# Kernel optimization log

Hardware: AMD Instinct MI355X
Metric: run time of the kernel (lower is better)

The kernel has to match this reference:

```python
import jax, jax.numpy as jnp
import numpy as np

N_ITEM_TYPE = 18
N_ITEM_FEAT = 11
N_TYPE_HIDDEN = 32
N_ITEM_HIDDEN = 128
BS, NA, NI = 32, 128, 128


def setup_inputs() -> dict:
    key = jax.random.key(0)
    k1, k2, k3, k4 = jax.random.split(key, 4)
    item_type = jax.random.randint(k1, (BS, NA, NI), 0, N_ITEM_TYPE, dtype=jnp.int64)
    item = jax.random.normal(k2, (BS, NA, NI, N_ITEM_FEAT), dtype=jnp.float32)
    emb = jax.random.normal(k3, (N_ITEM_TYPE, N_TYPE_HIDDEN), dtype=jnp.float32)
    W = jax.random.normal(k4, (N_TYPE_HIDDEN + N_ITEM_FEAT, N_ITEM_HIDDEN), dtype=jnp.float32) * 0.1
    b = jnp.zeros((N_ITEM_HIDDEN,), dtype=jnp.float32)
    return {"item_type": item_type, "item": item, "emb": emb, "W": W, "b": b}


def reference(item_type, item, emb, W, b):
    # embedding gather: [bs, na, ni, 32]
    h_type = emb[item_type]
    # concat features: [bs, na, ni, 43]
    h = jnp.concatenate([h_type, item], axis=-1)
    # Linear + ReLU: [bs, na, ni, n_item_hidden]
    h = jax.nn.relu(jnp.einsum("bnif,fh->bnih", h, W) + b)
    # max-pool over item axis: [bs, na, n_item_hidden]
    return jnp.max(h, axis=2)
```

## Files before the change

### kernel.cpp

```cpp
#include <hip/hip_runtime.h>
#include <hip/hip_bf16.h>
#include <stdint.h>


#define NITEM 128
#define NFEAT 11
#define NTH   32
#define NH    128
#define KREAL 43
#define KSTEPS 3

typedef __attribute__((ext_vector_type(8))) _Float16 half8;
typedef __attribute__((ext_vector_type(16))) float   f32x16;

__global__ __launch_bounds__(64) void prep_b(const float* __restrict__ W,
                                             _Float16* __restrict__ Bpre) {
    const int frag = blockIdx.x;
    const int kk   = frag >> 2;
    const int n    = frag & 3;
    const int lane = threadIdx.x;
    const int col  = n * 32 + (lane & 31);
    const int k0   = kk * 16 + (lane >> 5) * 8;
    half8 pk;
    #pragma unroll
    for (int q = 0; q < 8; ++q) {
        const int k = k0 + q;
        pk[q] = (_Float16)((k < KREAL) ? W[k * NH + col] : 0.0f);
    }
    ((half8*)Bpre)[frag * 64 + lane] = pk;
}

__global__ __launch_bounds__(256, 3) void item_encoder(
    const int*      __restrict__ item_type,
    const float*    __restrict__ item,
    const float*    __restrict__ emb,
    const _Float16* __restrict__ Bpre,
    const float*    __restrict__ bias,
    float*          __restrict__ out)
{
    __shared__ _Float16 Alds[NITEM][64];
    __shared__ float    partial[4][NH];

    const int bn   = blockIdx.x;
    const int t    = threadIdx.x;
    const int lane = t & 63;
    const int w    = t >> 6;
    const int l31  = lane & 31;
    const int lhi  = lane >> 5;

    half8 bf[KSTEPS][4];
    #pragma unroll
    for (int kk = 0; kk < KSTEPS; ++kk)
        #pragma unroll
        for (int n = 0; n < 4; ++n)
            bf[kk][n] = ((const half8*)Bpre)[(kk * 4 + n) * 64 + lane];

    const int*   tyrow = item_type + bn * NITEM;
    const float* itrow = item + (size_t)bn * NITEM * NFEAT;

    #pragma unroll
    for (int j = 0; j < 3; ++j) {
        const int idx = j * 256 + t;
        const int kb  = idx >> 7;
        const int row = idx & 127;
        half8 pk;
        if (kb < 4) {
            const int    ty = tyrow[row];
            const float4 e0 = *(const float4*)(emb + ty * NTH + kb * 8);
            const float4 e1 = *(const float4*)(emb + ty * NTH + kb * 8 + 4);
            pk[0] = (_Float16)e0.x; pk[1] = (_Float16)e0.y;
            pk[2] = (_Float16)e0.z; pk[3] = (_Float16)e0.w;
            pk[4] = (_Float16)e1.x; pk[5] = (_Float16)e1.y;
            pk[6] = (_Float16)e1.z; pk[7] = (_Float16)e1.w;
        } else if (kb == 4) {
            const float* p = itrow + row * NFEAT;
            #pragma unroll
            for (int q = 0; q < 8; ++q) pk[q] = (_Float16)p[q];
        } else {
            const float* p = itrow + row * NFEAT + 8;
            #pragma unroll
            for (int q = 0; q < 8; ++q) pk[q] = (_Float16)((q < 3) ? p[q] : 0.0f);
        }
        ((half8*)&Alds[row][0])[kb ^ (row & 7)] = pk;
    }

    __syncthreads();

    f32x16 acc[4];
    #pragma unroll
    for (int n = 0; n < 4; ++n)
        #pragma unroll
        for (int r = 0; r < 16; ++r) acc[n][r] = 0.0f;

    const int arow = w * 32 + l31;
    #pragma unroll
    for (int kk = 0; kk < KSTEPS; ++kk) {
        const int blk = kk * 2 + lhi;
        const half8 af = ((const half8*)&Alds[arow][0])[blk ^ (arow & 7)];
        #pragma unroll
        for (int n = 0; n < 4; ++n)
            acc[n] = __builtin_amdgcn_mfma_f32_32x32x16_f16(af, bf[kk][n], acc[n], 0, 0, 0);
    }

    #pragma unroll
    for (int n = 0; n < 4; ++n) {
        float m = acc[n][0];
        #pragma unroll
        for (int r = 1; r < 16; ++r) m = fmaxf(m, acc[n][r]);
        m = fmaxf(m, __shfl_xor(m, 32));
        m = fmaxf(m + bias[n * 32 + l31], 0.0f);
        if (lane < 32) partial[w][n * 32 + l31] = m;
    }

    __syncthreads();

    if (t < NH) {
        float m = fmaxf(fmaxf(partial[0][t], partial[1][t]),
                        fmaxf(partial[2][t], partial[3][t]));
        out[(size_t)bn * NH + t] = m;
    }
}

extern "C" void kernel_launch(void* const* d_in, const int* in_sizes, int n_in,
                              void* d_out, int out_size, void* d_ws, size_t ws_size,
                              hipStream_t stream) {
    const int*   item_type = (const int*)  d_in[0];
    const float* item      = (const float*)d_in[1];
    const float* emb       = (const float*)d_in[2];
    const float* W         = (const float*)d_in[3];
    const float* bias      = (const float*)d_in[4];
    float*       out       = (float*)d_out;
    _Float16*    Bpre      = (_Float16*)d_ws;

    prep_b<<<12, 64, 0, stream>>>(W, Bpre);
    item_encoder<<<32 * 128, 256, 0, stream>>>(item_type, item, emb, Bpre, bias, out);
}
```

Baseline: 95.75 us.

## Process four rows per block with coalesced float4 slab staging

Each block now handles four (batch, agent) rows. It stages the whole item-feature slab and the type indices into LDS with coalesced float4/int4 loads. MFMA A fragments are then built straight in registers from the emb gather and the LDS slab, using packed fp16 conversion, so the swizzled fp16 LDS tile is gone. The goal is to replace the strided per-element global feature loads and cut the per-block launch and B-fragment load overhead. In exchange, each block uses more LDS, occupancy drops from 3 to 2 blocks per CU, there are fewer blocks in the grid, and the four rows inside a block run serially.

Measured after the change: 91.07 us. -4.9%, faster.

```diff
diff --git a/kernel.cpp b/kernel.cpp
--- a/kernel.cpp
+++ b/kernel.cpp
@@ -3,15 +3,20 @@
 #include <stdint.h>
 
 
-#define NITEM 128
-#define NFEAT 11
-#define NTH   32
-#define NH    128
-#define KREAL 43
+#define NITEM  128
+#define NFEAT  11
+#define NTH    32
+#define NH     128
+#define KREAL  43
 #define KSTEPS 3
+#define BNPB   4
+#define SLABDW (NITEM * NFEAT)
 
-typedef __attribute__((ext_vector_type(8))) _Float16 half8;
-typedef __attribute__((ext_vector_type(16))) float   f32x16;
+typedef __attribute__((ext_vector_type(8)))  _Float16 half8;
+typedef __attribute__((ext_vector_type(2)))  __fp16   fp16x2;
+typedef __attribute__((ext_vector_type(16))) float    f32x16;
+
+union H8 { half8 h8; fp16x2 h2[4]; };
 
 __global__ __launch_bounds__(64) void prep_b(const float* __restrict__ W,
                                              _Float16* __restrict__ Bpre) {
@@ -30,7 +35,7 @@
     ((half8*)Bpre)[frag * 64 + lane] = pk;
 }
 
-__global__ __launch_bounds__(256, 3) void item_encoder(
+__global__ __launch_bounds__(256, 2) void item_encoder(
     const int*      __restrict__ item_type,
     const float*    __restrict__ item,
     const float*    __restrict__ emb,
@@ -38,15 +43,16 @@
     const float*    __restrict__ bias,
     float*          __restrict__ out)
 {
-    __shared__ _Float16 Alds[NITEM][64];
-    __shared__ float    partial[4][NH];
+    __shared__ float slab[BNPB * SLABDW];
+    __shared__ int   typs[BNPB * NITEM];
+    __shared__ float partial[BNPB][4][NH];
 
-    const int bn   = blockIdx.x;
     const int t    = threadIdx.x;
     const int lane = t & 63;
     const int w    = t >> 6;
     const int l31  = lane & 31;
     const int lhi  = lane >> 5;
+    const int bn0  = blockIdx.x * BNPB;
 
     half8 bf[KSTEPS][4];
     #pragma unroll
@@ -55,69 +61,90 @@
         for (int n = 0; n < 4; ++n)
             bf[kk][n] = ((const half8*)Bpre)[(kk * 4 + n) * 64 + lane];
 
-    const int*   tyrow = item_type + bn * NITEM;
-    const float* itrow = item + (size_t)bn * NITEM * NFEAT;
+    {
+        const float4* gsl = (const float4*)(item + (size_t)bn0 * SLABDW);
+        float4*       lsl = (float4*)slab;
+        #pragma unroll
+        for (int j = 0; j < 5; ++j) lsl[t + 256 * j] = gsl[t + 256 * j];
+        if (t < 128) lsl[1280 + t] = gsl[1280 + t];
+        if (t < 128)
+            ((int4*)typs)[t] = ((const int4*)(item_type + (size_t)bn0 * NITEM))[t];
+    }
+    __syncthreads();
 
+    const int r = w * 32 + l31;
+    float bias4[4];
     #pragma unroll
-    for (int j = 0; j < 3; ++j) {
-        const int idx = j * 256 + t;
-        const int kb  = idx >> 7;
-        const int row = idx & 127;
-        half8 pk;
-        if (kb < 4) {
-            const int    ty = tyrow[row];
-            const float4 e0 = *(const float4*)(emb + ty * NTH + kb * 8);
-            const float4 e1 = *(const float4*)(emb + ty * NTH + kb * 8 + 4);
-            pk[0] = (_Float16)e0.x; pk[1] = (_Float16)e0.y;
-            pk[2] = (_Float16)e0.z; pk[3] = (_Float16)e0.w;
-            pk[4] = (_Float16)e1.x; pk[5] = (_Float16)e1.y;
-            pk[6] = (_Float16)e1.z; pk[7] = (_Float16)e1.w;
-        } else if (kb == 4) {
-            const float* p = itrow + row * NFEAT;
+    for (int n = 0; n < 4; ++n) bias4[n] = bias[n * 32 + l31];
+
+    #pragma unroll 1
+    for (int b = 0; b < BNPB; ++b) {
+        const int    ty = typs[b * NITEM + r];
+        const float* eb = emb + ty * NTH;
+
+        const float4 e0 = *(const float4*)(eb + lhi * 8);
+        const float4 e1 = *(const float4*)(eb + lhi * 8 + 4);
+        const float4 e2 = *(const float4*)(eb + 16 + lhi * 8);
+        const float4 e3 = *(const float4*)(eb + 16 + lhi * 8 + 4);
+
+        H8 a0, a1, a2;
+        a0.h2[0] = __builtin_amdgcn_cvt_pkrtz(e0.x, e0.y);
+        a0.h2[1] = __builtin_amdgcn_cvt_pkrtz(e0.z, e0.w);
+        a0.h2[2] = __builtin_amdgcn_cvt_pkrtz(e1.x, e1.y);
+        a0.h2[3] = __builtin_amdgcn_cvt_pkrtz(e1.z, e1.w);
+        a1.h2[0] = __builtin_amdgcn_cvt_pkrtz(e2.x, e2.y);
+        a1.h2[1] = __builtin_amdgcn_cvt_pkrtz(e2.z, e2.w);
+        a1.h2[2] = __builtin_amdgcn_cvt_pkrtz(e3.x, e3.y);
+        a1.h2[3] = __builtin_amdgcn_cvt_pkrtz(e3.z, e3.w);
+
+        const float* sp = slab + b * SLABDW + r * NFEAT;
+        float fv[8];
+        #pragma unroll
+        for (int q = 0; q < 8; ++q) {
+            const int f  = lhi * 8 + q;
+            const bool ok = (f < NFEAT);
+            const float x = sp[ok ? f : 0];
+            fv[q] = ok ? x : 0.0f;
+        }
+        a2.h2[0] = __builtin_amdgcn_cvt_pkrtz(fv[0], fv[1]);
+        a2.h2[1] = __builtin_amdgcn_cvt_pkrtz(fv[2], fv[3]);
+        a2.h2[2] = __builtin_amdgcn_cvt_pkrtz(fv[4], fv[5]);
+        a2.h2[3] = __builtin_amdgcn_cvt_pkrtz(fv[6], fv[7]);
+
+        f32x16 acc[4];
+        #pragma unroll
+        for (int n = 0; n < 4; ++n)
             #pragma unroll
-            for (int q = 0; q < 8; ++q) pk[q] = (_Float16)p[q];
-        } else {
-            const float* p = itrow + row * NFEAT + 8;
+            for (int rr = 0; rr < 16; ++rr) acc[n][rr] = 0.0f;
+
+        #pragma unroll
+        for (int n = 0; n < 4; ++n) acc[n] = __builtin_amdgcn_mfma_f32_32x32x16_f16(a0.h8, bf[0][n], acc[n], 0, 0, 0);
+        #pragma unroll
+        for (int n = 0; n < 4; ++n) acc[n] = __builtin_amdgcn_mfma_f32_32x32x16_f16(a1.h8, bf[1][n], acc[n], 0, 0, 0);
+        #pragma unroll
+        for (int n = 0; n < 4; ++n) acc[n] = __builtin_amdgcn_mfma_f32_32x32x16_f16(a2.h8, bf[2][n], acc[n], 0, 0, 0);
+
+        #pragma unroll
+        for (int n = 0; n < 4; ++n) {
+            float m = acc[n][0];
             #pragma unroll
-            for (int q = 0; q < 8; ++q) pk[q] = (_Float16)((q < 3) ? p[q] : 0.0f);
+            for (int rr = 1; rr < 16; ++rr) m = fmaxf(m, acc[n][rr]);
+            m = fmaxf(m, __shfl_xor(m, 32));
+            m = fmaxf(m + bias4[n], 0.0f);
+            if (lane < 32) partial[b][w][n * 32 + l31] = m;
         }
-        ((half8*)&Alds[row][0])[kb ^ (row & 7)] = pk;
     }
 
     __syncthreads();
 
-    f32x16 acc[4];
     #pragma unroll
-    for (int n = 0; n < 4; ++n)
-        #pragma unroll
-        for (int r = 0; r < 16; ++r) acc[n][r] = 0.0f;
-
-    const int arow = w * 32 + l31;
-    #pragma unroll
-    for (int kk = 0; kk < KSTEPS; ++kk) {
-        const int blk = kk * 2 + lhi;
-        const half8 af = ((const half8*)&Alds[arow][0])[blk ^ (arow & 7)];
-        #pragma unroll
-        for (int n = 0; n < 4; ++n)
-            acc[n] = __builtin_amdgcn_mfma_f32_32x32x16_f16(af, bf[kk][n], acc[n], 0, 0, 0);
-    }
-
-    #pragma unroll
-    for (int n = 0; n < 4; ++n) {
-        float m = acc[n][0];
-        #pragma unroll
-        for (int r = 1; r < 16; ++r) m = fmaxf(m, acc[n][r]);
-        m = fmaxf(m, __shfl_xor(m, 32));
-        m = fmaxf(m + bias[n * 32 + l31], 0.0f);
-        if (lane < 32) partial[w][n * 32 + l31] = m;
-    }
-
-    __syncthreads();
-
-    if (t < NH) {
-        float m = fmaxf(fmaxf(partial[0][t], partial[1][t]),
-                        fmaxf(partial[2][t], partial[3][t]));
-        out[(size_t)bn * NH + t] = m;
+    for (int jj = 0; jj < 2; ++jj) {
+        const int idx = t + 256 * jj;
+        const int b   = idx >> 7;
+        const int col = idx & 127;
+        float m = fmaxf(fmaxf(partial[b][0][col], partial[b][1][col]),
+                        fmaxf(partial[b][2][col], partial[b][3][col]));
+        out[(size_t)(bn0 + b) * NH + col] = m;
     }
 }
 
@@ -133,5 +160,5 @@
     _Float16*    Bpre      = (_Float16*)d_ws;
 
     prep_b<<<12, 64, 0, stream>>>(W, Bpre);
-    item_encoder<<<32 * 128, 256, 0, stream>>>(item_type, item, emb, Bpre, bias, out);
+    item_encoder<<<(32 * 128) / BNPB, 256, 0, stream>>>(item_type, item, emb, Bpre, bias, out);
 }
```
